# Performance work log

Measured on AMD Instinct MI355X. Metric: run time of the kernel, lower is better.

## Reference

```python
import jax, jax.numpy as jnp
import numpy as np
from jax import lax

B, LATENT, SEQ, HID, OUT = 4096, 128, 512, 32, 64


def setup_inputs() -> dict:
    key = jax.random.key(0)
    ks = jax.random.split(key, 9)
    s = 1.0 / np.sqrt(HID)  # PyTorch-style init scale
    f32 = jnp.float32
    return {
        "z": jax.random.normal(ks[0], (B, LATENT), f32),
        "init_W": jax.random.uniform(ks[1], (HID, LATENT), f32, -s, s),
        "init_b": jax.random.uniform(ks[2], (HID,), f32, -s, s),
        "W_ih": jax.random.uniform(ks[3], (4 * HID, HID), f32, -s, s),
        "W_hh": jax.random.uniform(ks[4], (4 * HID, HID), f32, -s, s),
        "b_ih": jax.random.uniform(ks[5], (4 * HID,), f32, -s, s),
        "b_hh": jax.random.uniform(ks[6], (4 * HID,), f32, -s, s),
        "out_W": jax.random.uniform(ks[7], (OUT, HID), f32, -s, s),
        "out_b": jax.random.uniform(ks[8], (OUT,), f32, -s, s),
    }


def reference(z, init_W, init_b, W_ih, W_hh, b_ih, b_hh, out_W, out_b):
    # init_fc: z -> h0 (num_layers=1); cell starts at zero
    h0 = z @ init_W.T + init_b  # [B, H]
    c0 = jnp.zeros_like(h0)

    # x_in is all zeros, so the input-to-hidden term is a constant bias;
    # compute it once (keeps W_ih in the graph, matmul with zeros == 0).
    x_zero = jnp.zeros((z.shape[0], W_ih.shape[1]), z.dtype)
    gate_const = x_zero @ W_ih.T + b_ih + b_hh  # [B, 4H]

    def step(carry, _):
        h, c = carry
        gates = h @ W_hh.T + gate_const  # [B, 4H], PyTorch gate order i,f,g,o
        i, f, g, o = jnp.split(gates, 4, axis=-1)
        i = jax.nn.sigmoid(i)
        f = jax.nn.sigmoid(f)
        g = jnp.tanh(g)
        o = jax.nn.sigmoid(o)
        c = f * c + i * g
        h = o * jnp.tanh(c)
        return (h, c), h

    _, hs = lax.scan(step, (h0, c0), None, length=SEQ)  # [T, B, H]
    out = jnp.transpose(hs, (1, 0, 2))  # [B, T, H] (batch_first)
    y = out @ out_W.T + out_b  # [B, T, OUT]
    return y
```

## Files before the change

### kernel.cpp

```cpp
#include <hip/hip_runtime.h>


#define B_SZ   4096
#define LATENT 128
#define SEQ    512
#define HID    32
#define OUT_N  64
#define ROWS   16
#define LSW    40

typedef _Float16 f16x8 __attribute__((ext_vector_type(8)));
typedef float    f32x4 __attribute__((ext_vector_type(4)));

__device__ __forceinline__ float fexp2(float x) { return __builtin_amdgcn_exp2f(x); }
__device__ __forceinline__ float frcp(float x)  { return __builtin_amdgcn_rcpf(x); }
__device__ __forceinline__ float sigm(float x) {
    return frcp(1.f + fexp2(-1.44269504088896341f * x));
}
__device__ __forceinline__ float tanh_f(float x) {
    return fmaf(-2.f, frcp(1.f + fexp2(2.88539008177792681f * x)), 1.f);
}
__device__ __forceinline__ f16x8 cvt8(const float* p) {
    f16x8 r;
#pragma unroll
    for (int i = 0; i < 8; i++) r[i] = (_Float16)p[i];
    return r;
}
__device__ __forceinline__ void lds_barrier() {
    asm volatile("s_waitcnt lgkmcnt(0)\n\ts_barrier" ::: "memory");
}

__global__ __launch_bounds__(256)
void lstm_mfma4(const float* __restrict__ z,
                const float* __restrict__ init_W,
                const float* __restrict__ init_b,
                const float* __restrict__ W_hh,
                const float* __restrict__ b_ih,
                const float* __restrict__ b_hh,
                const float* __restrict__ out_W,
                const float* __restrict__ out_b,
                float* __restrict__ y)
{
    __shared__ __align__(16) _Float16 hst[2][ROWS * LSW];

    const int tid  = threadIdx.x;
    const int w    = tid >> 6;
    const int lane = tid & 63;
    const int n_   = lane & 15;
    const int kb   = lane >> 4;
    const int jj   = w >> 1;
    const int p2   = w & 1;
    const int rbase = blockIdx.x * ROWS;

    f16x8 bhh[4], bow;
    f32x4 bacc[4], oacc;
#pragma unroll
    for (int m = 0; m < 4; m++) {
        int g = (2 * m + jj) * 16 + n_;
        bhh[m] = cvt8(W_hh + (size_t)g * HID + kb * 8);
        float b = b_ih[g] + b_hh[g];
        bacc[m] = (f32x4){b, b, b, b};
    }
    {
        int col = w * 16 + n_;
        bow = cvt8(out_W + (size_t)col * HID + kb * 8);
        float b = out_b[col];
        oacc = (f32x4){b, b, b, b};
    }

#pragma unroll
    for (int i = 0; i < 2; i++) {
        int e = tid + 256 * i;
        int m = e >> 5, j = e & 31;
        const float4* zp = (const float4*)(z + (size_t)(rbase + m) * LATENT);
        const float4* wp = (const float4*)(init_W + (size_t)j * LATENT);
        float acc = init_b[j];
#pragma unroll
        for (int k = 0; k < LATENT / 4; k++) {
            float4 a4 = zp[k], b4 = wp[k];
            acc = fmaf(a4.x, b4.x, acc); acc = fmaf(a4.y, b4.y, acc);
            acc = fmaf(a4.z, b4.z, acc); acc = fmaf(a4.w, b4.w, acc);
        }
        hst[0][m * LSW + j] = (_Float16)acc;
    }
    __syncthreads();

    float c2[2] = {0.f, 0.f};

    f16x8 a = *(const f16x8*)&hst[0][n_ * LSW + kb * 8];

    float* yb = y + (size_t)(rbase + kb * 4) * SEQ * OUT_N + w * 16 + n_;

    int p = 0;
    for (int t = 0; t < SEQ; t++) {
        f32x4 acc[4];
#pragma unroll
        for (int m = 0; m < 4; m++)
            acc[m] = __builtin_amdgcn_mfma_f32_16x16x32_f16(a, bhh[m], bacc[m], 0, 0, 0);

#pragma unroll
        for (int r2 = 0; r2 < 2; r2++) {
            int r = 2 * p2 + r2;
            float gi = sigm(acc[0][r]);
            float gf = sigm(acc[1][r]);
            float gg = tanh_f(acc[2][r]);
            float go = sigm(acc[3][r]);
            float cn = fmaf(gf, c2[r2], gi * gg);
            c2[r2] = cn;
            float hn = go * tanh_f(cn);
            hst[p ^ 1][(kb * 4 + r) * LSW + jj * 16 + n_] = (_Float16)hn;
        }

        lds_barrier();

        a = *(const f16x8*)&hst[p ^ 1][n_ * LSW + kb * 8];
        f32x4 py = __builtin_amdgcn_mfma_f32_16x16x32_f16(a, bow, oacc, 0, 0, 0);
#pragma unroll
        for (int r = 0; r < 4; r++)
            yb[(size_t)r * SEQ * OUT_N + (size_t)t * OUT_N] = py[r];

        p ^= 1;
    }
}

extern "C" void kernel_launch(void* const* d_in, const int* in_sizes, int n_in,
                              void* d_out, int out_size, void* d_ws, size_t ws_size,
                              hipStream_t stream) {
    const float* z      = (const float*)d_in[0];
    const float* init_W = (const float*)d_in[1];
    const float* init_b = (const float*)d_in[2];
    const float* W_hh   = (const float*)d_in[4];
    const float* b_ih   = (const float*)d_in[5];
    const float* b_hh   = (const float*)d_in[6];
    const float* out_W  = (const float*)d_in[7];
    const float* out_b  = (const float*)d_in[8];
    float* yout = (float*)d_out;

    lstm_mfma4<<<B_SZ / ROWS, 256, 0, stream>>>(z, init_W, init_b, W_hh, b_ih, b_hh,
                                                out_W, out_b, yout);
}
```

Before: 691.7 us.

## Transpose MFMA operands so outputs store as float4 and hidden exchange packs

Swaps the MFMA A/B operands so each lane holds 4 consecutive output columns for one batch row. The y stores become a single 16-byte vector store per step instead of four scattered scalar stores. The hidden-state exchange now writes one packed 32-bit pair per lane into a double-buffered LDS array and reads it back as four dwords, with K permuted to match. This cuts LDS and global store instruction counts in the serial recurrence, at the cost of extra setup shuffles and a two-step unrolled loop.

Result: faster. 666.4 us (-3.7%).

```diff
diff --git a/kernel.cpp b/kernel.cpp
--- a/kernel.cpp
+++ b/kernel.cpp
@@ -10,6 +10,7 @@
 #define LSW    40
 
 typedef _Float16 f16x8 __attribute__((ext_vector_type(8)));
+typedef _Float16 f16x4 __attribute__((ext_vector_type(4)));
 typedef float    f32x4 __attribute__((ext_vector_type(4)));
 
 __device__ __forceinline__ float fexp2(float x) { return __builtin_amdgcn_exp2f(x); }
@@ -20,28 +21,23 @@
 __device__ __forceinline__ float tanh_f(float x) {
     return fmaf(-2.f, frcp(1.f + fexp2(2.88539008177792681f * x)), 1.f);
 }
-__device__ __forceinline__ f16x8 cvt8(const float* p) {
-    f16x8 r;
-#pragma unroll
-    for (int i = 0; i < 8; i++) r[i] = (_Float16)p[i];
-    return r;
-}
 __device__ __forceinline__ void lds_barrier() {
     asm volatile("s_waitcnt lgkmcnt(0)\n\ts_barrier" ::: "memory");
 }
 
 __global__ __launch_bounds__(256)
-void lstm_mfma4(const float* __restrict__ z,
-                const float* __restrict__ init_W,
-                const float* __restrict__ init_b,
-                const float* __restrict__ W_hh,
-                const float* __restrict__ b_ih,
-                const float* __restrict__ b_hh,
-                const float* __restrict__ out_W,
-                const float* __restrict__ out_b,
-                float* __restrict__ y)
+void lstm_tr4(const float* __restrict__ z,
+              const float* __restrict__ init_W,
+              const float* __restrict__ init_b,
+              const float* __restrict__ W_hh,
+              const float* __restrict__ b_ih,
+              const float* __restrict__ b_hh,
+              const float* __restrict__ out_W,
+              const float* __restrict__ out_b,
+              float* __restrict__ y)
 {
-    __shared__ __align__(16) _Float16 hst[2][ROWS * LSW];
+    __shared__ __align__(16) _Float16 hst[ROWS * LSW];
+    __shared__ unsigned int hx[2][4][64];
 
     const int tid  = threadIdx.x;
     const int w    = tid >> 6;
@@ -52,20 +48,40 @@
     const int p2   = w & 1;
     const int rbase = blockIdx.x * ROWS;
 
-    f16x8 bhh[4], bow;
-    f32x4 bacc[4], oacc;
+    f16x8 wf[4];
+    f32x4 bacc[4];
 #pragma unroll
     for (int m = 0; m < 4; m++) {
-        int g = (2 * m + jj) * 16 + n_;
-        bhh[m] = cvt8(W_hh + (size_t)g * HID + kb * 8);
-        float b = b_ih[g] + b_hh[g];
-        bacc[m] = (f32x4){b, b, b, b};
+        int g = 2 * m + jj;
+        const float* row = W_hh + (size_t)(16 * g + n_) * HID;
+        f16x8 v;
+#pragma unroll
+        for (int rr = 0; rr < 4; rr++) {
+            v[rr]     = (_Float16)row[4 * kb + rr];
+            v[4 + rr] = (_Float16)row[4 * kb + 16 + rr];
+        }
+        wf[m] = v;
+        f32x4 b;
+#pragma unroll
+        for (int r = 0; r < 4; r++) {
+            int G = 16 * g + 4 * kb + r;
+            b[r] = b_ih[G] + b_hh[G];
+        }
+        bacc[m] = b;
     }
+    f16x8 owf;
+    f32x4 oacc;
     {
-        int col = w * 16 + n_;
-        bow = cvt8(out_W + (size_t)col * HID + kb * 8);
-        float b = out_b[col];
-        oacc = (f32x4){b, b, b, b};
+        const float* row = out_W + (size_t)(16 * w + n_) * HID;
+        f16x8 v;
+#pragma unroll
+        for (int rr = 0; rr < 4; rr++) {
+            v[rr]     = (_Float16)row[4 * kb + rr];
+            v[4 + rr] = (_Float16)row[4 * kb + 16 + rr];
+        }
+        owf = v;
+#pragma unroll
+        for (int r = 0; r < 4; r++) oacc[r] = out_b[16 * w + 4 * kb + r];
     }
 
 #pragma unroll
@@ -81,45 +97,59 @@
             acc = fmaf(a4.x, b4.x, acc); acc = fmaf(a4.y, b4.y, acc);
             acc = fmaf(a4.z, b4.z, acc); acc = fmaf(a4.w, b4.w, acc);
         }
-        hst[0][m * LSW + j] = (_Float16)acc;
+        hst[m * LSW + j] = (_Float16)acc;
     }
     __syncthreads();
 
+    f16x8 a;
+    {
+        f16x4 lo = *(const f16x4*)&hst[n_ * LSW + 4 * kb];
+        f16x4 hi = *(const f16x4*)&hst[n_ * LSW + 4 * kb + 16];
+#pragma unroll
+        for (int r = 0; r < 4; r++) { a[r] = lo[r]; a[4 + r] = hi[r]; }
+    }
+
     float c2[2] = {0.f, 0.f};
 
-    f16x8 a = *(const f16x8*)&hst[0][n_ * LSW + kb * 8];
+    float* yb = y + (size_t)(rbase + n_) * SEQ * OUT_N + 16 * w + 4 * kb;
 
-    float* yb = y + (size_t)(rbase + kb * 4) * SEQ * OUT_N + w * 16 + n_;
+    for (int t = 0; t < SEQ; t += 2) {
+#pragma unroll
+        for (int u = 0; u < 2; u++) {
+            f32x4 acc[4];
+#pragma unroll
+            for (int m = 0; m < 4; m++)
+                acc[m] = __builtin_amdgcn_mfma_f32_16x16x32_f16(wf[m], a, bacc[m], 0, 0, 0);
 
-    int p = 0;
-    for (int t = 0; t < SEQ; t++) {
-        f32x4 acc[4];
+            unsigned int pk;
+            {
+                _Float16 hh[2];
 #pragma unroll
-        for (int m = 0; m < 4; m++)
-            acc[m] = __builtin_amdgcn_mfma_f32_16x16x32_f16(a, bhh[m], bacc[m], 0, 0, 0);
+                for (int r2 = 0; r2 < 2; r2++) {
+                    int r = 2 * p2 + r2;
+                    float gi = sigm(acc[0][r]);
+                    float gf = sigm(acc[1][r]);
+                    float gg = tanh_f(acc[2][r]);
+                    float go = sigm(acc[3][r]);
+                    float cn = fmaf(gf, c2[r2], gi * gg);
+                    c2[r2] = cn;
+                    hh[r2] = (_Float16)(go * tanh_f(cn));
+                }
+                union { _Float16 h[2]; unsigned int u32; } cv;
+                cv.h[0] = hh[0]; cv.h[1] = hh[1];
+                pk = cv.u32;
+            }
+            hx[u][w][lane] = pk;
+            lds_barrier();
 
+            union { f16x8 v; unsigned int u32[4]; } nv;
 #pragma unroll
-        for (int r2 = 0; r2 < 2; r2++) {
-            int r = 2 * p2 + r2;
-            float gi = sigm(acc[0][r]);
-            float gf = sigm(acc[1][r]);
-            float gg = tanh_f(acc[2][r]);
-            float go = sigm(acc[3][r]);
-            float cn = fmaf(gf, c2[r2], gi * gg);
-            c2[r2] = cn;
-            float hn = go * tanh_f(cn);
-            hst[p ^ 1][(kb * 4 + r) * LSW + jj * 16 + n_] = (_Float16)hn;
+            for (int q = 0; q < 4; q++) nv.u32[q] = hx[u][q][lane];
+            a = nv.v;
+
+            f32x4 py = __builtin_amdgcn_mfma_f32_16x16x32_f16(owf, a, oacc, 0, 0, 0);
+            *(f32x4*)(yb + (size_t)(t + u) * OUT_N) = py;
         }
-
-        lds_barrier();
-
-        a = *(const f16x8*)&hst[p ^ 1][n_ * LSW + kb * 8];
-        f32x4 py = __builtin_amdgcn_mfma_f32_16x16x32_f16(a, bow, oacc, 0, 0, 0);
-#pragma unroll
-        for (int r = 0; r < 4; r++)
-            yb[(size_t)r * SEQ * OUT_N + (size_t)t * OUT_N] = py[r];
-
-        p ^= 1;
     }
 }
 
@@ -136,6 +166,6 @@
     const float* out_b  = (const float*)d_in[8];
     float* yout = (float*)d_out;
 
-    lstm_mfma4<<<B_SZ / ROWS, 256, 0, stream>>>(z, init_W, init_b, W_hh, b_ih, b_hh,
-                                                out_W, out_b, yout);
+    lstm_tr4<<<B_SZ / ROWS, 256, 0, stream>>>(z, init_W, init_b, W_hh, b_ih, b_hh,
+                                              out_W, out_b, yout);
 }
```
